# Optimization experiments

Hardware: AMD Instinct MI355X
Metric: run time of the kernel (lower is better)

The kernel has to match this reference:

```python
import jax, jax.numpy as jnp
import numpy as np

DIM = 2048
THRESH = 0.33

def _ternary(w):
    # sign() with dead zone: {-1, 0, +1}; detached from grad (matches torch.no_grad)
    return jax.lax.stop_gradient(jnp.where(jnp.abs(w) < THRESH, 0.0, jnp.sign(w)))

def _bitlinear(x, w, b):
    # F.linear(x, ternary_w, bias): x @ ternary_w.T + b
    return jnp.einsum('bsd,od->bso', x, _ternary(w)) + b

def setup_inputs() -> dict:
    key = jax.random.key(0)
    ks = jax.random.split(key, 6)
    B, S, D = 8, 2048, DIM
    x = jax.random.normal(ks[0], (B, S, D), dtype=jnp.float32)
    h_prev = jax.random.normal(ks[1], (B, S, D), dtype=jnp.float32)
    # BitLinear reset_parameters: uniform(-1, 1); bias zeros
    wf = jax.random.uniform(ks[2], (D, D), minval=-1.0, maxval=1.0, dtype=jnp.float32)
    wc = jax.random.uniform(ks[3], (D, D), minval=-1.0, maxval=1.0, dtype=jnp.float32)
    wg = jax.random.uniform(ks[4], (D, D), minval=-1.0, maxval=1.0, dtype=jnp.float32)
    wo = jax.random.uniform(ks[5], (D, D), minval=-1.0, maxval=1.0, dtype=jnp.float32)
    bf = jnp.zeros((D,), dtype=jnp.float32)
    bc = jnp.zeros((D,), dtype=jnp.float32)
    bg = jnp.zeros((D,), dtype=jnp.float32)
    bo = jnp.zeros((D,), dtype=jnp.float32)
    return {"x": x, "h_prev": h_prev, "wf": wf, "bf": bf, "wc": wc, "bc": bc,
            "wg": wg, "bg": bg, "wo": wo, "bo": bo}

def reference(x, h_prev, wf, bf, wc, bc, wg, bg, wo, bo):
    f = jax.nn.sigmoid(_bitlinear(x, wf, bf))
    c = jax.nn.silu(_bitlinear(x, wc, bc))
    h = f * h_prev + (1.0 - f) * c
    g = jax.nn.sigmoid(_bitlinear(x, wg, bg))
    o = _bitlinear(g * h, wo, bo)
    return (o, h)
```

## Files before the change

### kernel.cpp

```cpp
#include <hip/hip_runtime.h>
#include <hip/hip_bf16.h>
#include <cstdint>

#define DIM   2048
#define MROWS 16384
#define NH    64
#define PLANE (MROWS * (size_t)DIM)

typedef __bf16 bf16x8 __attribute__((ext_vector_type(8)));
typedef float  f32x4  __attribute__((ext_vector_type(4)));
typedef unsigned short u16;
typedef unsigned int   u32;

#define BARRIER() asm volatile("s_barrier" ::: "memory")
#define WAITVM(N) asm volatile("s_waitcnt vmcnt(" #N ")" ::: "memory")


__device__ __forceinline__ u16 ternary_bits(float w) {
    u32 u = __float_as_uint(w);
    u16 s = (u16)((u >> 16) & 0x8000u);
    return (__builtin_fabsf(w) < 0.33f) ? (u16)0 : (u16)(0x3F80u | s);
}

__device__ __forceinline__ u16 f2bf_rne(float f) {
    u32 u = __float_as_uint(f);
    u32 r = (u + 0x7FFFu + ((u >> 16) & 1u)) >> 16;
    return (u16)r;
}

__device__ __forceinline__ float bf2f(u16 v) {
    u32 u = ((u32)v) << 16;
    return __uint_as_float(u);
}

__device__ __forceinline__ void gload16(const void* g, void* l) {
    __builtin_amdgcn_global_load_lds(
        (const __attribute__((address_space(1))) void*)g,
        (__attribute__((address_space(3))) void*)l,
        16, 0, 0);
}


__global__ void prep_weights(const float* __restrict__ wf, const float* __restrict__ wc,
                             const float* __restrict__ wg, const float* __restrict__ wo,
                             u16* __restrict__ out) {
    const float* srcs[4] = {wf, wc, wg, wo};
    const float* src = srcs[blockIdx.y];
    u16* dst = out + (size_t)blockIdx.y * (DIM * DIM);
    int e = (blockIdx.x * 256 + threadIdx.x) * 8;
    float4 v0 = *(const float4*)(src + e);
    float4 v1 = *(const float4*)(src + e + 4);
    ushort4 o0, o1;
    o0.x = ternary_bits(v0.x); o0.y = ternary_bits(v0.y);
    o0.z = ternary_bits(v0.z); o0.w = ternary_bits(v0.w);
    o1.x = ternary_bits(v1.x); o1.y = ternary_bits(v1.y);
    o1.z = ternary_bits(v1.z); o1.w = ternary_bits(v1.w);
    *(ushort4*)(dst + e)     = o0;
    *(ushort4*)(dst + e + 4) = o1;
}

__global__ void cast_x(const float* __restrict__ x, u16* __restrict__ xb) {
    size_t e = ((size_t)blockIdx.x * 256 + threadIdx.x) * 8;
    float4 v0 = *(const float4*)(x + e);
    float4 v1 = *(const float4*)(x + e + 4);
    ushort4 o0, o1;
    o0.x = f2bf_rne(v0.x); o0.y = f2bf_rne(v0.y);
    o0.z = f2bf_rne(v0.z); o0.w = f2bf_rne(v0.w);
    o1.x = f2bf_rne(v1.x); o1.y = f2bf_rne(v1.y);
    o1.z = f2bf_rne(v1.z); o1.w = f2bf_rne(v1.w);
    *(ushort4*)(xb + e)     = o0;
    *(ushort4*)(xb + e + 4) = o1;
}


__global__ __launch_bounds__(512) void gemm1p(
    const u16* __restrict__ xb,
    const u16* __restrict__ wt,
    u16* __restrict__ pf,
    u16* __restrict__ pc,
    u16* __restrict__ pg)
{
    __shared__ __align__(16) u16 lds[3 * 16384];

    const int tid  = threadIdx.x;
    const int lane = tid & 63;
    const int wave = tid >> 6;
    const int wr   = wave >> 2;
    const int wcq  = wave & 3;

    const int bid   = blockIdx.x;
    const int swz   = (bid & 7) * 192 + (bid >> 3);
    const int mtile = swz & 63;
    const int ntile = swz >> 6;
    const int brow  = mtile * 256;
    const int bcol  = ntile * 256;

    const int srow = tid >> 2;
    const int gc4  = (tid & 3) ^ ((tid >> 3) & 3);
    const int ldst = tid * 8;

    const int fr  = lane & 15;
    const int hi  = lane >> 4;
    const int csw = (hi ^ ((fr >> 1) & 3)) * 8;

    f32x4 accL[8][2] = {};
    f32x4 accH[8][2] = {};

    const u16* aSrc0 = xb + (size_t)(brow + srow) * DIM;
    const u16* aSrc1 = xb + (size_t)(brow + 128 + srow) * DIM;
    const u16* bSrc0 = wt + (size_t)(bcol + srow) * DIM;
    const u16* bSrc1 = wt + (size_t)(bcol + 128 + srow) * DIM;

    auto issueA = [&](int so, int k0) {
        gload16(aSrc0 + k0 + gc4 * 8, (u16*)&lds[so + ldst]);
        gload16(aSrc1 + k0 + gc4 * 8, (u16*)&lds[so + 4096 + ldst]);
    };
    auto issueB = [&](int so, int k0) {
        gload16(bSrc0 + k0 + gc4 * 8, (u16*)&lds[so + 8192 + ldst]);
        gload16(bSrc1 + k0 + gc4 * 8, (u16*)&lds[so + 12288 + ldst]);
    };

    auto rdA = [&](int so, bf16x8 (&a)[8]) {
        #pragma unroll
        for (int mi = 0; mi < 8; ++mi)
            a[mi] = *(const bf16x8*)(&lds[so + (wr * 128 + mi * 16 + fr) * 32 + csw]);
    };
    auto rdBL = [&](int so, bf16x8 (&b)[2]) {
        #pragma unroll
        for (int jn = 0; jn < 2; ++jn)
            b[jn] = *(const bf16x8*)(&lds[so + 8192 + (wcq * 64 + jn * 16 + fr) * 32 + csw]);
    };
    auto rdBH = [&](int so, bf16x8 (&b)[2]) {
        #pragma unroll
        for (int jn = 0; jn < 2; ++jn)
            b[jn] = *(const bf16x8*)(&lds[so + 8192 + (wcq * 64 + (2 + jn) * 16 + fr) * 32 + csw]);
    };
    auto mfma2 = [&](bf16x8 (&a)[8], bf16x8 (&b)[2], f32x4 (&c)[8][2]) {
        __builtin_amdgcn_s_setprio(1);
        #pragma unroll
        for (int jn = 0; jn < 2; ++jn)
            #pragma unroll
            for (int mi = 0; mi < 8; ++mi)
                c[mi][jn] = __builtin_amdgcn_mfma_f32_16x16x32_bf16(a[mi], b[jn], c[mi][jn], 0, 0, 0);
        __builtin_amdgcn_s_setprio(0);
    };

    int so0 = 0, so1 = 16384, so2 = 32768;

    bf16x8 aP[8], bLP[2], aQ[8], bLQ[2], bH[2];

    issueA(so0, 0); issueB(so0, 0);
    issueA(so1, 32); issueB(so1, 32);
    WAITVM(4);
    BARRIER();
    rdA(so0, aP); rdBL(so0, bLP);

    auto step = [&](int h, bf16x8 (&aC)[8], bf16x8 (&bLC)[2],
                    bf16x8 (&aN)[8], bf16x8 (&bLN)[2]) {
        const int kn = (h + 2) * 32;
        rdBH(so0, bH);
        issueA(so2, kn);
        mfma2(aC, bLC, accL);
        WAITVM(2);
        BARRIER();
        rdA(so1, aN); rdBL(so1, bLN);
        issueB(so2, kn);
        mfma2(aC, bH, accH);
        BARRIER();
        int t = so0; so0 = so1; so1 = so2; so2 = t;
    };

    #pragma unroll 1
    for (int h = 0; h < NH - 2; h += 2) {
        step(h,     aP, bLP, aQ, bLQ);
        step(h + 1, aQ, bLQ, aP, bLP);
    }
    {
        rdBH(so0, bH);
        mfma2(aP, bLP, accL);
        WAITVM(0);
        BARRIER();
        rdA(so1, aQ); rdBL(so1, bLQ);
        mfma2(aP, bH, accH);
        BARRIER();
        int t = so0; so0 = so1; so1 = so2; so2 = t;
    }
    {
        rdBH(so0, bH);
        mfma2(aQ, bLQ, accL);
        mfma2(aQ, bH, accH);
    }

    const int gate = bcol >> 11;
    const int colb = bcol & 2047;
    u16* outp = (gate == 0) ? pf : (gate == 1) ? pc : pg;

    auto epi2 = [&](int nbase, f32x4 (&c)[8][2]) {
        #pragma unroll
        for (int jn = 0; jn < 2; ++jn) {
            const int col = colb + wcq * 64 + (nbase + jn) * 16 + fr;
            #pragma unroll
            for (int mi = 0; mi < 8; ++mi)
                #pragma unroll
                for (int j = 0; j < 4; ++j)
                    outp[(size_t)(brow + wr * 128 + mi * 16 + hi * 4 + j) * DIM + col] =
                        f2bf_rne(c[mi][jn][j]);
        }
    };
    epi2(0, accL);
    epi2(2, accH);
}


__global__ __launch_bounds__(256) void fuse_gates(
    const u16* __restrict__ pf, const u16* __restrict__ pc, const u16* __restrict__ pg,
    const float* __restrict__ bfv_, const float* __restrict__ bcv_, const float* __restrict__ bgv_,
    const float* __restrict__ hprev,
    float* __restrict__ hout,
    u16* __restrict__ gh)
{
    #pragma unroll 1
    for (int it = 0; it < 4; ++it) {
        const size_t u = (size_t)blockIdx.x * 256 + threadIdx.x + (size_t)it * 1048576;
        const size_t e = u * 8;
        const int col = (int)(e & 2047);

        ushort4 f0 = *(const ushort4*)(pf + e), f1 = *(const ushort4*)(pf + e + 4);
        ushort4 c0 = *(const ushort4*)(pc + e), c1 = *(const ushort4*)(pc + e + 4);
        ushort4 g0 = *(const ushort4*)(pg + e), g1 = *(const ushort4*)(pg + e + 4);
        float4 hp0 = *(const float4*)(hprev + e), hp1 = *(const float4*)(hprev + e + 4);
        float4 bf0 = *(const float4*)(bfv_ + col), bf1 = *(const float4*)(bfv_ + col + 4);
        float4 bc0 = *(const float4*)(bcv_ + col), bc1 = *(const float4*)(bcv_ + col + 4);
        float4 bg0 = *(const float4*)(bgv_ + col), bg1 = *(const float4*)(bgv_ + col + 4);

        float4 h0, h1;
        ushort4 o0, o1;

        #define DO_ELEM(V, HP, PF, PC, PG, BF, BC, BG, OUT)                   \
        {                                                                      \
            float pfv = bf2f(PF) + (BF);                                       \
            float pcv = bf2f(PC) + (BC);                                       \
            float pgv = bf2f(PG) + (BG);                                       \
            float f  = 1.f / (1.f + __expf(-pfv));                             \
            float cc = pcv / (1.f + __expf(-pcv));                             \
            float g  = 1.f / (1.f + __expf(-pgv));                             \
            float hh = f * (HP) + (1.f - f) * cc;                              \
            V = hh;                                                            \
            OUT = f2bf_rne(g * hh);                                            \
        }
        DO_ELEM(h0.x, hp0.x, f0.x, c0.x, g0.x, bf0.x, bc0.x, bg0.x, o0.x);
        DO_ELEM(h0.y, hp0.y, f0.y, c0.y, g0.y, bf0.y, bc0.y, bg0.y, o0.y);
        DO_ELEM(h0.z, hp0.z, f0.z, c0.z, g0.z, bf0.z, bc0.z, bg0.z, o0.z);
        DO_ELEM(h0.w, hp0.w, f0.w, c0.w, g0.w, bf0.w, bc0.w, bg0.w, o0.w);
        DO_ELEM(h1.x, hp1.x, f1.x, c1.x, g1.x, bf1.x, bc1.x, bg1.x, o1.x);
        DO_ELEM(h1.y, hp1.y, f1.y, c1.y, g1.y, bf1.y, bc1.y, bg1.y, o1.y);
        DO_ELEM(h1.z, hp1.z, f1.z, c1.z, g1.z, bf1.z, bc1.z, bg1.z, o1.z);
        DO_ELEM(h1.w, hp1.w, f1.w, c1.w, g1.w, bf1.w, bc1.w, bg1.w, o1.w);
        #undef DO_ELEM

        *(float4*)(hout + e)     = h0;
        *(float4*)(hout + e + 4) = h1;
        *(ushort4*)(gh + e)      = o0;
        *(ushort4*)(gh + e + 4)  = o1;
    }
}


__global__ __launch_bounds__(512) void gemm2(
    const u16* __restrict__ gh,
    const u16* __restrict__ wot,
    const float* __restrict__ bov_,
    float* __restrict__ oout)
{
    __shared__ __align__(16) u16 lds[3 * 16384];

    const int tid  = threadIdx.x;
    const int lane = tid & 63;
    const int wave = tid >> 6;
    const int wr   = wave >> 2;
    const int wcq  = wave & 3;

    const int bid  = blockIdx.x;
    const int swz  = (bid & 7) * 64 + (bid >> 3);
    const int brow = (swz & 63) * 256;
    const int bcol = (swz >> 6) * 256;

    const int srow = tid >> 2;
    const int gc4  = (tid & 3) ^ ((tid >> 3) & 3);
    const int ldst = tid * 8;

    const int fr  = lane & 15;
    const int hi  = lane >> 4;
    const int csw = (hi ^ ((fr >> 1) & 3)) * 8;

    f32x4 accL[8][2] = {};
    f32x4 accH[8][2] = {};

    const u16* aSrc0 = gh  + (size_t)(brow + srow) * DIM;
    const u16* aSrc1 = gh  + (size_t)(brow + 128 + srow) * DIM;
    const u16* bSrc0 = wot + (size_t)(bcol + srow) * DIM;
    const u16* bSrc1 = wot + (size_t)(bcol + 128 + srow) * DIM;

    auto issueA = [&](int so, int k0) {
        gload16(aSrc0 + k0 + gc4 * 8, (u16*)&lds[so + ldst]);
        gload16(aSrc1 + k0 + gc4 * 8, (u16*)&lds[so + 4096 + ldst]);
    };
    auto issueB = [&](int so, int k0) {
        gload16(bSrc0 + k0 + gc4 * 8, (u16*)&lds[so + 8192 + ldst]);
        gload16(bSrc1 + k0 + gc4 * 8, (u16*)&lds[so + 12288 + ldst]);
    };

    auto rdA = [&](int so, bf16x8 (&a)[8]) {
        #pragma unroll
        for (int mi = 0; mi < 8; ++mi)
            a[mi] = *(const bf16x8*)(&lds[so + (wr * 128 + mi * 16 + fr) * 32 + csw]);
    };
    auto rdBL = [&](int so, bf16x8 (&b)[2]) {
        #pragma unroll
        for (int jn = 0; jn < 2; ++jn)
            b[jn] = *(const bf16x8*)(&lds[so + 8192 + (wcq * 64 + jn * 16 + fr) * 32 + csw]);
    };
    auto rdBH = [&](int so, bf16x8 (&b)[2]) {
        #pragma unroll
        for (int jn = 0; jn < 2; ++jn)
            b[jn] = *(const bf16x8*)(&lds[so + 8192 + (wcq * 64 + (2 + jn) * 16 + fr) * 32 + csw]);
    };
    auto mfma2 = [&](bf16x8 (&a)[8], bf16x8 (&b)[2], f32x4 (&c)[8][2]) {
        __builtin_amdgcn_s_setprio(1);
        #pragma unroll
        for (int jn = 0; jn < 2; ++jn)
            #pragma unroll
            for (int mi = 0; mi < 8; ++mi)
                c[mi][jn] = __builtin_amdgcn_mfma_f32_16x16x32_bf16(a[mi], b[jn], c[mi][jn], 0, 0, 0);
        __builtin_amdgcn_s_setprio(0);
    };

    int so0 = 0, so1 = 16384, so2 = 32768;

    bf16x8 aP[8], bLP[2], aQ[8], bLQ[2], bH[2];

    issueA(so0, 0); issueB(so0, 0);
    issueA(so1, 32); issueB(so1, 32);
    WAITVM(4);
    BARRIER();
    rdA(so0, aP); rdBL(so0, bLP);

    auto step = [&](int h, bf16x8 (&aC)[8], bf16x8 (&bLC)[2],
                    bf16x8 (&aN)[8], bf16x8 (&bLN)[2]) {
        const int kn = (h + 2) * 32;
        rdBH(so0, bH);
        issueA(so2, kn);
        mfma2(aC, bLC, accL);
        WAITVM(2);
        BARRIER();
        rdA(so1, aN); rdBL(so1, bLN);
        issueB(so2, kn);
        mfma2(aC, bH, accH);
        BARRIER();
        int t = so0; so0 = so1; so1 = so2; so2 = t;
    };

    #pragma unroll 1
    for (int h = 0; h < NH - 2; h += 2) {
        step(h,     aP, bLP, aQ, bLQ);
        step(h + 1, aQ, bLQ, aP, bLP);
    }
    {
        rdBH(so0, bH);
        mfma2(aP, bLP, accL);
        WAITVM(0);
        BARRIER();
        rdA(so1, aQ); rdBL(so1, bLQ);
        mfma2(aP, bH, accH);
        BARRIER();
        int t = so0; so0 = so1; so1 = so2; so2 = t;
    }
    {
        rdBH(so0, bH);
        mfma2(aQ, bLQ, accL);
        mfma2(aQ, bH, accH);
    }

    auto epi2 = [&](int nbase, f32x4 (&c)[8][2]) {
        #pragma unroll
        for (int jn = 0; jn < 2; ++jn) {
            const int col = bcol + wcq * 64 + (nbase + jn) * 16 + fr;
            const float bov = bov_[col];
            #pragma unroll
            for (int mi = 0; mi < 8; ++mi)
                #pragma unroll
                for (int j = 0; j < 4; ++j)
                    oout[(size_t)(brow + wr * 128 + mi * 16 + hi * 4 + j) * DIM + col] = c[mi][jn][j] + bov;
        }
    };
    epi2(0, accL);
    epi2(2, accH);
}

extern "C" void kernel_launch(void* const* d_in, const int* in_sizes, int n_in,
                              void* d_out, int out_size, void* d_ws, size_t ws_size,
                              hipStream_t stream) {
    const float* x  = (const float*)d_in[0];
    const float* hp = (const float*)d_in[1];
    const float* wf = (const float*)d_in[2];
    const float* bf = (const float*)d_in[3];
    const float* wc = (const float*)d_in[4];
    const float* bc = (const float*)d_in[5];
    const float* wg = (const float*)d_in[6];
    const float* bg = (const float*)d_in[7];
    const float* wo = (const float*)d_in[8];
    const float* bo = (const float*)d_in[9];

    float* o_out = (float*)d_out;
    float* h_out = o_out + PLANE;

    u16* w_t  = (u16*)d_ws;
    u16* x_bf = (u16*)((char*)d_ws + 33554432);
    u16* gh   = (u16*)((char*)d_ws + 100663296);

    u16* p_f = (u16*)o_out;
    u16* p_c = p_f + PLANE;

    prep_weights<<<dim3(2048, 4), 256, 0, stream>>>(wf, wc, wg, wo, w_t);
    cast_x<<<dim3(16384), 256, 0, stream>>>(x, x_bf);
    gemm1p<<<dim3(1536), 512, 0, stream>>>(x_bf, w_t, p_f, p_c, gh);
    fuse_gates<<<dim3(4096), 256, 0, stream>>>(p_f, p_c, gh, bf, bc, bg, hp, h_out, gh);
    gemm2<<<dim3(512), 512, 0, stream>>>(gh, w_t + 3 * (size_t)DIM * DIM, bo, o_out);
}
```

Measured before the change: 830.0 us.

## Unify GEMMs into templated kernel with 8-phase double-buffered K=64 pipeline

```diff
diff --git a/kernel.cpp b/kernel.cpp
--- a/kernel.cpp
+++ b/kernel.cpp
@@ -4,7 +4,6 @@
 
 #define DIM   2048
 #define MROWS 16384
-#define NH    64
 #define PLANE (MROWS * (size_t)DIM)
 
 typedef __bf16 bf16x8 __attribute__((ext_vector_type(8)));
@@ -73,142 +72,167 @@
 }
 
 
-__global__ __launch_bounds__(512) void gemm1p(
-    const u16* __restrict__ xb,
-    const u16* __restrict__ wt,
-    u16* __restrict__ pf,
-    u16* __restrict__ pc,
-    u16* __restrict__ pg)
+template<bool PRE>
+__global__ __launch_bounds__(512) void gemm8p(
+    const u16* __restrict__ Amat,
+    const u16* __restrict__ Wmat,
+    u16* __restrict__ pf, u16* __restrict__ pc, u16* __restrict__ pg,
+    const float* __restrict__ bias, float* __restrict__ oout)
 {
-    __shared__ __align__(16) u16 lds[3 * 16384];
+    __shared__ __align__(16) u16 lds[65536];
 
     const int tid  = threadIdx.x;
     const int lane = tid & 63;
     const int wave = tid >> 6;
-    const int wr   = wave >> 2;
-    const int wcq  = wave & 3;
-
-    const int bid   = blockIdx.x;
-    const int swz   = (bid & 7) * 192 + (bid >> 3);
-    const int mtile = swz & 63;
-    const int ntile = swz >> 6;
-    const int brow  = mtile * 256;
-    const int bcol  = ntile * 256;
-
-    const int srow = tid >> 2;
+    const int wm   = wave >> 2;
+    const int wn   = wave & 3;
+
+    const int CPX  = PRE ? 192 : 64;
+    const int swz  = (blockIdx.x & 7) * CPX + (blockIdx.x >> 3);
+    const int brow = (swz & 63) * 256;
+    const int bcol = (swz >> 6) * 256;
+
     const int gc4  = (tid & 3) ^ ((tid >> 3) & 3);
-    const int ldst = tid * 8;
-
-    const int fr  = lane & 15;
-    const int hi  = lane >> 4;
-    const int csw = (hi ^ ((fr >> 1) & 3)) * 8;
-
-    f32x4 accL[8][2] = {};
-    f32x4 accH[8][2] = {};
-
-    const u16* aSrc0 = xb + (size_t)(brow + srow) * DIM;
-    const u16* aSrc1 = xb + (size_t)(brow + 128 + srow) * DIM;
-    const u16* bSrc0 = wt + (size_t)(bcol + srow) * DIM;
-    const u16* bSrc1 = wt + (size_t)(bcol + 128 + srow) * DIM;
-
-    auto issueA = [&](int so, int k0) {
-        gload16(aSrc0 + k0 + gc4 * 8, (u16*)&lds[so + ldst]);
-        gload16(aSrc1 + k0 + gc4 * 8, (u16*)&lds[so + 4096 + ldst]);
-    };
-    auto issueB = [&](int so, int k0) {
-        gload16(bSrc0 + k0 + gc4 * 8, (u16*)&lds[so + 8192 + ldst]);
-        gload16(bSrc1 + k0 + gc4 * 8, (u16*)&lds[so + 12288 + ldst]);
-    };
-
-    auto rdA = [&](int so, bf16x8 (&a)[8]) {
+    const int fr   = lane & 15;
+    const int hi   = lane >> 4;
+    const int csw  = (hi ^ ((fr >> 1) & 3)) * 8;
+
+    f32x4 acc[8][4] = {};
+
+    const u16* aSrc = Amat + (size_t)(brow + (tid >> 2)) * DIM;
+    const u16* bSrc = Wmat + (size_t)(bcol + (tid >> 2)) * DIM;
+
+    auto stA = [&](int b, int h, int t) {
+        const int k0 = t * 64 + h * 32;
+        u16* dst = &lds[b * 32768 + h * 16384 + tid * 8];
+        gload16(aSrc + k0 + gc4 * 8, dst);
+        gload16(aSrc + (size_t)128 * DIM + k0 + gc4 * 8, dst + 4096);
+    };
+    auto stB = [&](int b, int h, int t) {
+        const int k0 = t * 64 + h * 32;
+        u16* dst = &lds[b * 32768 + h * 16384 + 8192 + tid * 8];
+        gload16(bSrc + k0 + gc4 * 8, dst);
+        gload16(bSrc + (size_t)128 * DIM + k0 + gc4 * 8, dst + 4096);
+    };
+
+    auto rdA = [&](int b, int h, bf16x8 (&a)[8]) {
+        const u16* p = &lds[b * 32768 + h * 16384];
         #pragma unroll
         for (int mi = 0; mi < 8; ++mi)
-            a[mi] = *(const bf16x8*)(&lds[so + (wr * 128 + mi * 16 + fr) * 32 + csw]);
-    };
-    auto rdBL = [&](int so, bf16x8 (&b)[2]) {
-        #pragma unroll
-        for (int jn = 0; jn < 2; ++jn)
-            b[jn] = *(const bf16x8*)(&lds[so + 8192 + (wcq * 64 + jn * 16 + fr) * 32 + csw]);
-    };
-    auto rdBH = [&](int so, bf16x8 (&b)[2]) {
-        #pragma unroll
-        for (int jn = 0; jn < 2; ++jn)
-            b[jn] = *(const bf16x8*)(&lds[so + 8192 + (wcq * 64 + (2 + jn) * 16 + fr) * 32 + csw]);
-    };
-    auto mfma2 = [&](bf16x8 (&a)[8], bf16x8 (&b)[2], f32x4 (&c)[8][2]) {
+            a[mi] = *(const bf16x8*)(p + (wm * 128 + mi * 16 + fr) * 32 + csw);
+    };
+    auto rdB = [&](int b, int h, int nh, bf16x8 (&bb)[2]) {
+        const u16* p = &lds[b * 32768 + h * 16384 + 8192];
+        #pragma unroll
+        for (int j = 0; j < 2; ++j)
+            bb[j] = *(const bf16x8*)(p + (wn * 64 + (nh * 2 + j) * 16 + fr) * 32 + csw);
+    };
+    auto mf = [&](bf16x8 (&a)[8], bf16x8 (&bb)[2], int nh) {
         __builtin_amdgcn_s_setprio(1);
         #pragma unroll
-        for (int jn = 0; jn < 2; ++jn)
+        for (int j = 0; j < 2; ++j)
             #pragma unroll
             for (int mi = 0; mi < 8; ++mi)
-                c[mi][jn] = __builtin_amdgcn_mfma_f32_16x16x32_bf16(a[mi], b[jn], c[mi][jn], 0, 0, 0);
+                acc[mi][nh * 2 + j] =
+                    __builtin_amdgcn_mfma_f32_16x16x32_bf16(a[mi], bb[j], acc[mi][nh * 2 + j], 0, 0, 0);
         __builtin_amdgcn_s_setprio(0);
     };
 
-    int so0 = 0, so1 = 16384, so2 = 32768;
-
-    bf16x8 aP[8], bLP[2], aQ[8], bLQ[2], bH[2];
-
-    issueA(so0, 0); issueB(so0, 0);
-    issueA(so1, 32); issueB(so1, 32);
-    WAITVM(4);
+    bf16x8 a[8], bb[2];
+
+    stA(0, 0, 0); stB(0, 0, 0);
+    stA(0, 1, 0); stB(0, 1, 0);
+    stA(1, 0, 1); stB(1, 0, 1);
+    WAITVM(8);
     BARRIER();
-    rdA(so0, aP); rdBL(so0, bLP);
-
-    auto step = [&](int h, bf16x8 (&aC)[8], bf16x8 (&bLC)[2],
-                    bf16x8 (&aN)[8], bf16x8 (&bLN)[2]) {
-        const int kn = (h + 2) * 32;
-        rdBH(so0, bH);
-        issueA(so2, kn);
-        mfma2(aC, bLC, accL);
-        WAITVM(2);
-        BARRIER();
-        rdA(so1, aN); rdBL(so1, bLN);
-        issueB(so2, kn);
-        mfma2(aC, bH, accH);
-        BARRIER();
-        int t = so0; so0 = so1; so1 = so2; so2 = t;
-    };
 
     #pragma unroll 1
-    for (int h = 0; h < NH - 2; h += 2) {
-        step(h,     aP, bLP, aQ, bLQ);
-        step(h + 1, aQ, bLQ, aP, bLP);
+    for (int t = 0; t < 30; ++t) {
+        const int b = t & 1, bn = b ^ 1;
+        rdA(b, 0, a); rdB(b, 0, 0, bb);
+        stA(bn, 1, t + 1);
+        BARRIER();
+        mf(a, bb, 0);
+        BARRIER();
+        rdB(b, 0, 1, bb);
+        stB(bn, 1, t + 1);
+        WAITVM(8);
+        BARRIER();
+        mf(a, bb, 1);
+        BARRIER();
+        rdA(b, 1, a); rdB(b, 1, 0, bb);
+        stA(b, 0, t + 2);
+        BARRIER();
+        mf(a, bb, 0);
+        BARRIER();
+        rdB(b, 1, 1, bb);
+        stB(b, 0, t + 2);
+        WAITVM(8);
+        BARRIER();
+        mf(a, bb, 1);
+        BARRIER();
     }
     {
-        rdBH(so0, bH);
-        mfma2(aP, bLP, accL);
+        rdA(0, 0, a); rdB(0, 0, 0, bb);
+        stA(1, 1, 31);
+        BARRIER(); mf(a, bb, 0); BARRIER();
+        rdB(0, 0, 1, bb);
+        stB(1, 1, 31);
+        WAITVM(8);
+        BARRIER(); mf(a, bb, 1); BARRIER();
+        rdA(0, 1, a); rdB(0, 1, 0, bb);
+        BARRIER(); mf(a, bb, 0); BARRIER();
+        rdB(0, 1, 1, bb);
+        WAITVM(4);
+        BARRIER(); mf(a, bb, 1); BARRIER();
+    }
+    {
+        rdA(1, 0, a); rdB(1, 0, 0, bb);
+        BARRIER(); mf(a, bb, 0); BARRIER();
+        rdB(1, 0, 1, bb);
         WAITVM(0);
-        BARRIER();
-        rdA(so1, aQ); rdBL(so1, bLQ);
-        mfma2(aP, bH, accH);
-        BARRIER();
-        int t = so0; so0 = so1; so1 = so2; so2 = t;
-    }
-    {
-        rdBH(so0, bH);
-        mfma2(aQ, bLQ, accL);
-        mfma2(aQ, bH, accH);
-    }
-
-    const int gate = bcol >> 11;
-    const int colb = bcol & 2047;
-    u16* outp = (gate == 0) ? pf : (gate == 1) ? pc : pg;
-
-    auto epi2 = [&](int nbase, f32x4 (&c)[8][2]) {
-        #pragma unroll
-        for (int jn = 0; jn < 2; ++jn) {
-            const int col = colb + wcq * 64 + (nbase + jn) * 16 + fr;
+        BARRIER(); mf(a, bb, 1); BARRIER();
+        rdA(1, 1, a); rdB(1, 1, 0, bb);
+        BARRIER(); mf(a, bb, 0); BARRIER();
+        rdB(1, 1, 1, bb);
+        mf(a, bb, 1);
+    }
+
+    if (PRE) {
+        BARRIER();
+        #pragma unroll
+        for (int mi = 0; mi < 8; ++mi)
+            #pragma unroll
+            for (int ni = 0; ni < 4; ++ni)
+                #pragma unroll
+                for (int j = 0; j < 4; ++j)
+                    lds[(wm * 128 + mi * 16 + hi * 4 + j) * 256 + wn * 64 + ni * 16 + fr] =
+                        f2bf_rne(acc[mi][ni][j]);
+        BARRIER();
+        const int gate = bcol >> 11;
+        const int colb = bcol & 2047;
+        u16* outp = (gate == 0) ? pf : (gate == 1) ? pc : pg;
+        const int rr = tid >> 5;
+        const int cc = (tid & 31) * 8;
+        #pragma unroll
+        for (int rg = 0; rg < 16; ++rg) {
+            const int row = rg * 16 + rr;
+            bf16x8 v = *(const bf16x8*)(&lds[row * 256 + cc]);
+            *(bf16x8*)(outp + (size_t)(brow + row) * DIM + colb + cc) = v;
+        }
+    } else {
+        #pragma unroll
+        for (int ni = 0; ni < 4; ++ni) {
+            const int col = bcol + wn * 64 + ni * 16 + fr;
+            const float bv = bias[col];
             #pragma unroll
             for (int mi = 0; mi < 8; ++mi)
                 #pragma unroll
                 for (int j = 0; j < 4; ++j)
-                    outp[(size_t)(brow + wr * 128 + mi * 16 + hi * 4 + j) * DIM + col] =
-                        f2bf_rne(c[mi][jn][j]);
+                    oout[(size_t)(brow + wm * 128 + mi * 16 + hi * 4 + j) * DIM + col] =
+                        acc[mi][ni][j] + bv;
         }
-    };
-    epi2(0, accL);
-    epi2(2, accH);
+    }
 }
 
 
@@ -265,138 +289,6 @@
     }
 }
 
-
-__global__ __launch_bounds__(512) void gemm2(
-    const u16* __restrict__ gh,
-    const u16* __restrict__ wot,
-    const float* __restrict__ bov_,
-    float* __restrict__ oout)
-{
-    __shared__ __align__(16) u16 lds[3 * 16384];
-
-    const int tid  = threadIdx.x;
-    const int lane = tid & 63;
-    const int wave = tid >> 6;
-    const int wr   = wave >> 2;
-    const int wcq  = wave & 3;
-
-    const int bid  = blockIdx.x;
-    const int swz  = (bid & 7) * 64 + (bid >> 3);
-    const int brow = (swz & 63) * 256;
-    const int bcol = (swz >> 6) * 256;
-
-    const int srow = tid >> 2;
-    const int gc4  = (tid & 3) ^ ((tid >> 3) & 3);
-    const int ldst = tid * 8;
-
-    const int fr  = lane & 15;
-    const int hi  = lane >> 4;
-    const int csw = (hi ^ ((fr >> 1) & 3)) * 8;
-
-    f32x4 accL[8][2] = {};
-    f32x4 accH[8][2] = {};
-
-    const u16* aSrc0 = gh  + (size_t)(brow + srow) * DIM;
-    const u16* aSrc1 = gh  + (size_t)(brow + 128 + srow) * DIM;
-    const u16* bSrc0 = wot + (size_t)(bcol + srow) * DIM;
-    const u16* bSrc1 = wot + (size_t)(bcol + 128 + srow) * DIM;
-
-    auto issueA = [&](int so, int k0) {
-        gload16(aSrc0 + k0 + gc4 * 8, (u16*)&lds[so + ldst]);
-        gload16(aSrc1 + k0 + gc4 * 8, (u16*)&lds[so + 4096 + ldst]);
-    };
-    auto issueB = [&](int so, int k0) {
-        gload16(bSrc0 + k0 + gc4 * 8, (u16*)&lds[so + 8192 + ldst]);
-        gload16(bSrc1 + k0 + gc4 * 8, (u16*)&lds[so + 12288 + ldst]);
-    };
-
-    auto rdA = [&](int so, bf16x8 (&a)[8]) {
-        #pragma unroll
-        for (int mi = 0; mi < 8; ++mi)
-            a[mi] = *(const bf16x8*)(&lds[so + (wr * 128 + mi * 16 + fr) * 32 + csw]);
-    };
-    auto rdBL = [&](int so, bf16x8 (&b)[2]) {
-        #pragma unroll
-        for (int jn = 0; jn < 2; ++jn)
-            b[jn] = *(const bf16x8*)(&lds[so + 8192 + (wcq * 64 + jn * 16 + fr) * 32 + csw]);
-    };
-    auto rdBH = [&](int so, bf16x8 (&b)[2]) {
-        #pragma unroll
-        for (int jn = 0; jn < 2; ++jn)
-            b[jn] = *(const bf16x8*)(&lds[so + 8192 + (wcq * 64 + (2 + jn) * 16 + fr) * 32 + csw]);
-    };
-    auto mfma2 = [&](bf16x8 (&a)[8], bf16x8 (&b)[2], f32x4 (&c)[8][2]) {
-        __builtin_amdgcn_s_setprio(1);
-        #pragma unroll
-        for (int jn = 0; jn < 2; ++jn)
-            #pragma unroll
-            for (int mi = 0; mi < 8; ++mi)
-                c[mi][jn] = __builtin_amdgcn_mfma_f32_16x16x32_bf16(a[mi], b[jn], c[mi][jn], 0, 0, 0);
-        __builtin_amdgcn_s_setprio(0);
-    };
-
-    int so0 = 0, so1 = 16384, so2 = 32768;
-
-    bf16x8 aP[8], bLP[2], aQ[8], bLQ[2], bH[2];
-
-    issueA(so0, 0); issueB(so0, 0);
-    issueA(so1, 32); issueB(so1, 32);
-    WAITVM(4);
-    BARRIER();
-    rdA(so0, aP); rdBL(so0, bLP);
-
-    auto step = [&](int h, bf16x8 (&aC)[8], bf16x8 (&bLC)[2],
-                    bf16x8 (&aN)[8], bf16x8 (&bLN)[2]) {
-        const int kn = (h + 2) * 32;
-        rdBH(so0, bH);
-        issueA(so2, kn);
-        mfma2(aC, bLC, accL);
-        WAITVM(2);
-        BARRIER();
-        rdA(so1, aN); rdBL(so1, bLN);
-        issueB(so2, kn);
-        mfma2(aC, bH, accH);
-        BARRIER();
-        int t = so0; so0 = so1; so1 = so2; so2 = t;
-    };
-
-    #pragma unroll 1
-    for (int h = 0; h < NH - 2; h += 2) {
-        step(h,     aP, bLP, aQ, bLQ);
-        step(h + 1, aQ, bLQ, aP, bLP);
-    }
-    {
-        rdBH(so0, bH);
-        mfma2(aP, bLP, accL);
-        WAITVM(0);
-        BARRIER();
-        rdA(so1, aQ); rdBL(so1, bLQ);
-        mfma2(aP, bH, accH);
-        BARRIER();
-        int t = so0; so0 = so1; so1 = so2; so2 = t;
-    }
-    {
-        rdBH(so0, bH);
-        mfma2(aQ, bLQ, accL);
-        mfma2(aQ, bH, accH);
-    }
-
-    auto epi2 = [&](int nbase, f32x4 (&c)[8][2]) {
-        #pragma unroll
-        for (int jn = 0; jn < 2; ++jn) {
-            const int col = bcol + wcq * 64 + (nbase + jn) * 16 + fr;
-            const float bov = bov_[col];
-            #pragma unroll
-            for (int mi = 0; mi < 8; ++mi)
-                #pragma unroll
-                for (int j = 0; j < 4; ++j)
-                    oout[(size_t)(brow + wr * 128 + mi * 16 + hi * 4 + j) * DIM + col] = c[mi][jn][j] + bov;
-        }
-    };
-    epi2(0, accL);
-    epi2(2, accH);
-}
-
 extern "C" void kernel_launch(void* const* d_in, const int* in_sizes, int n_in,
                               void* d_out, int out_size, void* d_ws, size_t ws_size,
                               hipStream_t stream) {
@@ -423,7 +315,8 @@
 
     prep_weights<<<dim3(2048, 4), 256, 0, stream>>>(wf, wc, wg, wo, w_t);
     cast_x<<<dim3(16384), 256, 0, stream>>>(x, x_bf);
-    gemm1p<<<dim3(1536), 512, 0, stream>>>(x_bf, w_t, p_f, p_c, gh);
+    gemm8p<true><<<dim3(1536), 512, 0, stream>>>(x_bf, w_t, p_f, p_c, gh, nullptr, nullptr);
     fuse_gates<<<dim3(4096), 256, 0, stream>>>(p_f, p_c, gh, bf, bc, bg, hp, h_out, gh);
-    gemm2<<<dim3(512), 512, 0, stream>>>(gh, w_t + 3 * (size_t)DIM * DIM, bo, o_out);
-}
+    gemm8p<false><<<dim3(512), 512, 0, stream>>>(gh, w_t + 3 * (size_t)DIM * DIM,
+                                                 nullptr, nullptr, nullptr, bo, o_out);
+}
```

Result: faster. 742.6 us (median of 2 runs) (-10.5%).
